# Kernel optimization log

Hardware: AMD Instinct MI355X
Metric: run time of the kernel (lower is better)

## Reference

```python
import jax, jax.numpy as jnp
import numpy as np

N = 262144      # total nodes in disjoint batch
E = 4194304     # total edges (COO)
G = 4096        # number of graphs
DIN = 1
CH = 32


def setup_inputs() -> dict:
    key = jax.random.key(0)
    ks = jax.random.split(key, 16)
    inp = {
        "x": jax.random.uniform(ks[0], (N, DIN), dtype=jnp.float32),
        "edge_src": jax.random.randint(ks[1], (E,), 0, N, dtype=jnp.int32),
        "edge_dst": jax.random.randint(ks[2], (E,), 0, N, dtype=jnp.int32),
        "edge_w": jax.random.uniform(ks[3], (E,), dtype=jnp.float32),  # normalized-adj values
        "seg": jnp.sort(jax.random.randint(ks[4], (N,), 0, G, dtype=jnp.int32)),
        "W1_1": jax.random.normal(ks[5], (DIN, CH), dtype=jnp.float32) * 0.5,
        "W2_1": jax.random.normal(ks[6], (DIN, CH), dtype=jnp.float32) * 0.5,
        "b1": jnp.zeros((CH,), jnp.float32),
        "W1_2": jax.random.normal(ks[7], (CH, CH), dtype=jnp.float32) * (1.0 / np.sqrt(CH)),
        "W2_2": jax.random.normal(ks[8], (CH, CH), dtype=jnp.float32) * (1.0 / np.sqrt(CH)),
        "b2": jnp.zeros((CH,), jnp.float32),
        "W1_3": jax.random.normal(ks[9], (CH, CH), dtype=jnp.float32) * (1.0 / np.sqrt(CH)),
        "W2_3": jax.random.normal(ks[10], (CH, CH), dtype=jnp.float32) * (1.0 / np.sqrt(CH)),
        "b3": jnp.zeros((CH,), jnp.float32),
        "Wd": jax.random.normal(ks[11], (CH, 1), dtype=jnp.float32) * (1.0 / np.sqrt(CH)),
        "bd": jnp.zeros((1,), jnp.float32),
    }
    return inp


def gcs_conv(x, src, dst, w, W1, W2, b):
    # GCSConv: out = relu(A_hat @ (x W1) + x W2 + b), A_hat sparse COO
    h = x @ W1                                   # [N, CH]
    msg = h[src] * w[:, None]                    # gather + edge weight [E, CH]
    agg = jax.ops.segment_sum(msg, dst, num_segments=N)  # scatter-add [N, CH]
    return jax.nn.relu(agg + x @ W2 + b)


def reference(x, edge_src, edge_dst, edge_w, seg,
              W1_1, W2_1, b1, W1_2, W2_2, b2, W1_3, W2_3, b3, Wd, bd):
    x = gcs_conv(x, edge_src, edge_dst, edge_w, W1_1, W2_1, b1)
    x = gcs_conv(x, edge_src, edge_dst, edge_w, W1_2, W2_2, b2)
    x = gcs_conv(x, edge_src, edge_dst, edge_w, W1_3, W2_3, b3)
    # GlobalAvgPool over graph segments
    sums = jax.ops.segment_sum(x, seg, num_segments=G)           # [G, CH]
    counts = jax.ops.segment_sum(jnp.ones((x.shape[0],), x.dtype), seg, num_segments=G)
    pooled = sums / jnp.maximum(counts, 1.0)[:, None]            # [G, CH]
    return jax.nn.sigmoid(pooled @ Wd + bd)                      # [G, 1]
```

## Files before the change

### kernel.cpp

```cpp
#include <hip/hip_runtime.h>
#include <hip/hip_bf16.h>

#define CH 32
#define BSHIFT 10
#define BNODES (1 << BSHIFT)
#define MAXBUK 256
#define P3_CHUNK 8192
#define NT 32
#define CAP 2048

__device__ __forceinline__ float bf_lo(unsigned int p) { return __int_as_float(p << 16); }
__device__ __forceinline__ float bf_hi(unsigned int p) { return __int_as_float(p & 0xffff0000u); }


__global__ void bucket_hist_kernel(const int* __restrict__ dst, int* __restrict__ bucketCount,
                                   int E, int nbuk) {
    __shared__ int h[MAXBUK];
    int tid = threadIdx.x;
    if (tid < nbuk) h[tid] = 0;
    __syncthreads();
    int stride = gridDim.x * blockDim.x;
    for (int e = blockIdx.x * blockDim.x + tid; e < E; e += stride)
        atomicAdd(&h[dst[e] >> BSHIFT], 1);
    __syncthreads();
    if (tid < nbuk && h[tid]) atomicAdd(&bucketCount[tid], h[tid]);
}

__global__ void bucket_scan_kernel(const int* __restrict__ bucketCount, int* __restrict__ bucketStart,
                                   int* __restrict__ bucketTail, int* __restrict__ row_start,
                                   int nbuk, int N, int E) {
    __shared__ int l[MAXBUK];
    int tid = threadIdx.x;
    int v = (tid < nbuk) ? bucketCount[tid] : 0;
    l[tid] = v;
    __syncthreads();
    for (int off = 1; off < MAXBUK; off <<= 1) {
        int t = (tid >= off) ? l[tid - off] : 0;
        __syncthreads();
        l[tid] += t;
        __syncthreads();
    }
    int ex = l[tid] - v;
    if (tid < nbuk) { bucketStart[tid] = ex; bucketTail[tid] = ex; }
    if (tid == nbuk - 1) bucketStart[nbuk] = ex + v;
    if (tid == 0) row_start[N] = E;
}

__global__ void bucket_scatter_kernel(const int* __restrict__ src, const int* __restrict__ dst,
                                      const float* __restrict__ w, int* __restrict__ bucketTail,
                                      int2* __restrict__ rec, int E, int nbuk) {
    __shared__ int cnt[MAXBUK], base[MAXBUK], offs[MAXBUK];
    int tid = threadIdx.x;
    int begin = blockIdx.x * P3_CHUNK;
    int end = min(begin + P3_CHUNK, E);
    if (tid < nbuk) cnt[tid] = 0;
    __syncthreads();
    for (int e = begin + tid; e < end; e += 256)
        atomicAdd(&cnt[dst[e] >> BSHIFT], 1);
    __syncthreads();
    if (tid < nbuk) {
        base[tid] = cnt[tid] ? atomicAdd(&bucketTail[tid], cnt[tid]) : 0;
        offs[tid] = 0;
    }
    __syncthreads();
    for (int e = begin + tid; e < end; e += 256) {
        int d = dst[e];
        int b = d >> BSHIFT;
        int p = base[b] + atomicAdd(&offs[b], 1);
        rec[p] = make_int2(src[e] | ((d & (BNODES - 1)) << 18), __float_as_int(w[e]));
    }
}

__global__ void local_csr_kernel(const int2* __restrict__ rec, const int* __restrict__ bucketStart,
                                 int* __restrict__ row_start, int2* __restrict__ colw, int N) {
    int b = blockIdx.x;
    int lo = bucketStart[b], hi = bucketStart[b + 1];
    int nodeBase = b << BSHIFT;
    int nNodes = min(BNODES, N - nodeBase);
    __shared__ int deg[BNODES];
    __shared__ int rs[BNODES];
    __shared__ int l[256];
    int tid = threadIdx.x;
    for (int i = tid; i < BNODES; i += 256) deg[i] = 0;
    __syncthreads();
    for (int j = lo + tid; j < hi; j += 256)
        atomicAdd(&deg[rec[j].x >> 18], 1);
    __syncthreads();
    int i0 = tid * 4;
    int v0 = deg[i0], v1 = deg[i0 + 1], v2 = deg[i0 + 2], v3 = deg[i0 + 3];
    int tsum = v0 + v1 + v2 + v3;
    l[tid] = tsum;
    __syncthreads();
    for (int off = 1; off < 256; off <<= 1) {
        int t = (tid >= off) ? l[tid - off] : 0;
        __syncthreads();
        l[tid] += t;
        __syncthreads();
    }
    int ex = l[tid] - tsum;
    rs[i0] = ex; rs[i0 + 1] = ex + v0; rs[i0 + 2] = ex + v0 + v1; rs[i0 + 3] = ex + v0 + v1 + v2;
    __syncthreads();
    for (int i = tid; i < nNodes; i += 256) row_start[nodeBase + i] = lo + rs[i];
    for (int i = tid; i < BNODES; i += 256) deg[i] = 0;
    __syncthreads();
    for (int j = lo + tid; j < hi; j += 256) {
        int2 r = rec[j];
        int dl = r.x >> 18;
        int p = lo + rs[dl] + atomicAdd(&deg[dl], 1);
        colw[p] = make_int2(r.x & 0x3FFFF, r.y);
    }
}

__global__ void l1_fused_kernel(const float* __restrict__ x,
                                const int* __restrict__ row_start, const int2* __restrict__ colw,
                                const float* __restrict__ W11, const float* __restrict__ W21,
                                const float* __restrict__ b1, const float* __restrict__ W12,
                                float* __restrict__ x1, __hip_bfloat16* __restrict__ h2, int N) {
    __shared__ float w1s[CH][CH];
    __shared__ float xs[8][CH + 1];
    int tid = threadIdx.x;
    for (int t = tid; t < CH * CH; t += 256) w1s[t >> 5][t & 31] = W12[t];
    int ln = tid >> 5, c = tid & 31;
    int node = blockIdx.x * 8 + ln;
    float s = 0.f, xv = 0.f;
    if (node < N) {
        xv = x[node];
        int lo = row_start[node], hi = row_start[node + 1];
        for (int j = lo + c; j < hi; j += 32) {
            int2 cw = colw[j];
            s += __int_as_float(cw.y) * x[cw.x];
        }
    }
    for (int m = 1; m < 32; m <<= 1) s += __shfl_xor(s, m);
    float x1v = 0.f;
    if (node < N) {
        x1v = fmaxf(fmaf(s, W11[c], fmaf(xv, W21[c], b1[c])), 0.f);
        x1[node * CH + c] = x1v;
    }
    xs[ln][c] = x1v;
    __syncthreads();
    if (node < N) {
        float a = 0.f;
#pragma unroll
        for (int k = 0; k < CH; k++) a = fmaf(xs[ln][k], w1s[k][c], a);
        h2[node * CH + c] = __float2bfloat16(a);
    }
}

__global__ void gemm_h_kernel(const float* __restrict__ xin, const float* __restrict__ W1,
                              __hip_bfloat16* __restrict__ h, int N) {
    __shared__ float w1s[CH][CH];
    __shared__ float xs[8][CH + 1];
    int tid = threadIdx.x;
    for (int t = tid; t < CH * CH; t += 256) w1s[t >> 5][t & 31] = W1[t];
    int ln = tid >> 5, c = tid & 31;
    int node = blockIdx.x * 8 + ln;
    float xv = (node < N) ? xin[node * CH + c] : 0.f;
    xs[ln][c] = xv;
    __syncthreads();
    if (node < N) {
        float a = 0.f;
#pragma unroll
        for (int k = 0; k < CH; k++) a = fmaf(xs[ln][k], w1s[k][c], a);
        h[node * CH + c] = __float2bfloat16(a);
    }
}

__global__ void gather_kernel(float* __restrict__ xio, const unsigned short* __restrict__ h,
                              const int* __restrict__ row_start, const int2* __restrict__ colw,
                              const float* __restrict__ W2, const float* __restrict__ b, int N) {
    __shared__ float w2s[CH][CH];
    __shared__ float xs[NT][CH + 1];
    __shared__ int2 cws[CAP];
    int tid = threadIdx.x;
    int nodeBase = blockIdx.x * NT;

    for (int t = tid; t < CH * CH; t += 256) w2s[t >> 5][t & 31] = W2[t];
    {
        int n = tid >> 5, c = tid & 31;
        for (int p = 0; p < NT / 8; p++) {
            int node = nodeBase + p * 8 + n;
            xs[p * 8 + n][c] = (node < N) ? xio[(size_t)node * CH + c] : 0.f;
        }
    }
    int tileEndNode = min(nodeBase + NT, N);
    int lo = row_start[min(nodeBase, N)];
    int hi = row_start[tileEndNode];
    int cnt = min(hi - lo, CAP);
    for (int t = tid; t < cnt; t += 256) cws[t] = colw[lo + t];
    __syncthreads();

    int grp = tid >> 4, l16 = tid & 15;
    int c0 = l16 * 2;
#pragma unroll
    for (int rep = 0; rep < NT / 16; rep++) {
        int nloc = rep * 16 + grp;
        int node = nodeBase + nloc;
        if (node >= N) continue;
        int ls = row_start[node], le = row_start[node + 1];
        float a0 = b[c0], a1 = b[c0 + 1];
#pragma unroll
        for (int k = 0; k < CH; k++) {
            float xk = xs[nloc][k];
            float2 wk = *reinterpret_cast<const float2*>(&w2s[k][c0]);
            a0 = fmaf(xk, wk.x, a0);
            a1 = fmaf(xk, wk.y, a1);
        }
        if (le - lo <= cnt) {
            int j = ls;
            for (; j + 4 <= le; j += 4) {
                int2 e0 = cws[j - lo], e1 = cws[j + 1 - lo], e2 = cws[j + 2 - lo], e3 = cws[j + 3 - lo];
                unsigned int p0 = *reinterpret_cast<const unsigned int*>(h + (size_t)e0.x * CH + c0);
                unsigned int p1 = *reinterpret_cast<const unsigned int*>(h + (size_t)e1.x * CH + c0);
                unsigned int p2 = *reinterpret_cast<const unsigned int*>(h + (size_t)e2.x * CH + c0);
                unsigned int p3 = *reinterpret_cast<const unsigned int*>(h + (size_t)e3.x * CH + c0);
                float w0 = __int_as_float(e0.y), w1 = __int_as_float(e1.y);
                float w2 = __int_as_float(e2.y), w3 = __int_as_float(e3.y);
                a0 = fmaf(w0, bf_lo(p0), a0); a1 = fmaf(w0, bf_hi(p0), a1);
                a0 = fmaf(w1, bf_lo(p1), a0); a1 = fmaf(w1, bf_hi(p1), a1);
                a0 = fmaf(w2, bf_lo(p2), a0); a1 = fmaf(w2, bf_hi(p2), a1);
                a0 = fmaf(w3, bf_lo(p3), a0); a1 = fmaf(w3, bf_hi(p3), a1);
            }
            for (; j < le; j++) {
                int2 e = cws[j - lo];
                unsigned int p = *reinterpret_cast<const unsigned int*>(h + (size_t)e.x * CH + c0);
                float wj = __int_as_float(e.y);
                a0 = fmaf(wj, bf_lo(p), a0); a1 = fmaf(wj, bf_hi(p), a1);
            }
        } else {
            for (int j = ls; j < le; j++) {
                int2 e = colw[j];
                unsigned int p = *reinterpret_cast<const unsigned int*>(h + (size_t)e.x * CH + c0);
                float wj = __int_as_float(e.y);
                a0 = fmaf(wj, bf_lo(p), a0); a1 = fmaf(wj, bf_hi(p), a1);
            }
        }
        float2 o = make_float2(fmaxf(a0, 0.f), fmaxf(a1, 0.f));
        *reinterpret_cast<float2*>(&xio[(size_t)node * CH + c0]) = o;
    }
}

__global__ void pool_head_kernel(const float* __restrict__ x3, const int* __restrict__ seg,
                                 const float* __restrict__ Wd, const float* __restrict__ bd,
                                 float* __restrict__ out, int N, int G) {
    int g = blockIdx.x;
    int tid = threadIdx.x;
    int lo = 0, hi = N;
    while (lo < hi) { int mid = (lo + hi) >> 1; if (seg[mid] < g) lo = mid + 1; else hi = mid; }
    int start = lo;
    hi = N;
    while (lo < hi) { int mid = (lo + hi) >> 1; if (seg[mid] < g + 1) lo = mid + 1; else hi = mid; }
    int end = lo;
    int half = tid >> 5, c = tid & 31;
    float s = 0.f;
    for (int n = start + half; n < end; n += 2) s += x3[(size_t)n * CH + c];
    s += __shfl_xor(s, 32);
    float t = s * Wd[c];
    for (int m = 1; m < 32; m <<= 1) t += __shfl_xor(t, m);
    if (tid == 0) {
        float cnt = fmaxf((float)(end - start), 1.f);
        float logit = t / cnt + bd[0];
        out[g] = 1.f / (1.f + expf(-logit));
    }
}

extern "C" void kernel_launch(void* const* d_in, const int* in_sizes, int n_in,
                              void* d_out, int out_size, void* d_ws, size_t ws_size,
                              hipStream_t stream) {
    const float* x        = (const float*)d_in[0];
    const int*   edge_src = (const int*)d_in[1];
    const int*   edge_dst = (const int*)d_in[2];
    const float* edge_w   = (const float*)d_in[3];
    const int*   seg      = (const int*)d_in[4];
    const float* W1_1 = (const float*)d_in[5];
    const float* W2_1 = (const float*)d_in[6];
    const float* b1   = (const float*)d_in[7];
    const float* W1_2 = (const float*)d_in[8];
    const float* W2_2 = (const float*)d_in[9];
    const float* b2   = (const float*)d_in[10];
    const float* W1_3 = (const float*)d_in[11];
    const float* W2_3 = (const float*)d_in[12];
    const float* b3   = (const float*)d_in[13];
    const float* Wd   = (const float*)d_in[14];
    const float* bd   = (const float*)d_in[15];
    float* out = (float*)d_out;

    const int N = in_sizes[0];
    const int E = in_sizes[1];
    const int G = out_size;
    (void)ws_size; (void)n_in;

    const int nbuk = (N + BNODES - 1) >> BSHIFT;

    const size_t NB = (size_t)N * CH;
    float*           xbuf      = (float*)d_ws;
    int2*            rec       = (int2*)d_ws;
    __hip_bfloat16*  h16       = (__hip_bfloat16*)(xbuf + NB);
    int*             row_start = (int*)(h16 + NB);
    int2*            colw      = (int2*)(row_start + (N + 8));
    int*             bucketCount = (int*)(colw + E);
    int*             bucketStart = bucketCount + MAXBUK;
    int*             bucketTail  = bucketStart + MAXBUK + 4;

    const int BLK = 256;

    hipMemsetAsync(bucketCount, 0, MAXBUK * sizeof(int), stream);
    bucket_hist_kernel<<<512, BLK, 0, stream>>>(edge_dst, bucketCount, E, nbuk);
    bucket_scan_kernel<<<1, BLK, 0, stream>>>(bucketCount, bucketStart, bucketTail, row_start, nbuk, N, E);
    bucket_scatter_kernel<<<(E + P3_CHUNK - 1) / P3_CHUNK, BLK, 0, stream>>>(
        edge_src, edge_dst, edge_w, bucketTail, rec, E, nbuk);
    local_csr_kernel<<<nbuk, BLK, 0, stream>>>(rec, bucketStart, row_start, colw, N);

    l1_fused_kernel<<<(N + 7) / 8, BLK, 0, stream>>>(x, row_start, colw,
                                                     W1_1, W2_1, b1, W1_2, xbuf, h16, N);
    gather_kernel<<<(N + NT - 1) / NT, BLK, 0, stream>>>(xbuf, (const unsigned short*)h16,
                                                         row_start, colw, W2_2, b2, N);
    gemm_h_kernel<<<(N + 7) / 8, BLK, 0, stream>>>(xbuf, W1_3, h16, N);
    gather_kernel<<<(N + NT - 1) / NT, BLK, 0, stream>>>(xbuf, (const unsigned short*)h16,
                                                         row_start, colw, W2_3, b3, N);

    pool_head_kernel<<<G, 64, 0, stream>>>(xbuf, seg, Wd, bd, out, N, G);
}
```

Measured before the change: 447.5 us.

## Store hidden features in FP8 and fuse next-layer GEMM into gather

Stores the per-node transformed features h in FP8 e4m3 instead of bf16, which halves the bytes fetched by the random per-edge gathers. The layer-2 gather kernel now also computes the layer-3 x@W1 product from its own outputs and writes it to a second h buffer, so the separate gemm_h kernel launch and its re-read of x go away. The edge-cache capacity CAP is lowered, which cuts shared memory and may raise occupancy. FP8 has far less mantissa than bf16, so accuracy drops and results could fail tolerance.

```diff
diff --git a/kernel.cpp b/kernel.cpp
--- a/kernel.cpp
+++ b/kernel.cpp
@@ -1,5 +1,6 @@
 #include <hip/hip_runtime.h>
 #include <hip/hip_bf16.h>
+#include <hip/hip_fp8.h>
 
 #define CH 32
 #define BSHIFT 10
@@ -7,10 +8,14 @@
 #define MAXBUK 256
 #define P3_CHUNK 8192
 #define NT 32
-#define CAP 2048
-
-__device__ __forceinline__ float bf_lo(unsigned int p) { return __int_as_float(p << 16); }
-__device__ __forceinline__ float bf_hi(unsigned int p) { return __int_as_float(p & 0xffff0000u); }
+#define CAP 1024
+
+__device__ __forceinline__ float fp8_to_f32(unsigned int b) {
+    __hip_fp8_e4m3 v; v.__x = (__hip_fp8_storage_t)b; return (float)v;
+}
+__device__ __forceinline__ unsigned char f32_to_fp8(float f) {
+    return (unsigned char)__hip_fp8_e4m3(f).__x;
+}
 
 
 __global__ void bucket_hist_kernel(const int* __restrict__ dst, int* __restrict__ bucketCount,
@@ -115,7 +120,7 @@
                                 const int* __restrict__ row_start, const int2* __restrict__ colw,
                                 const float* __restrict__ W11, const float* __restrict__ W21,
                                 const float* __restrict__ b1, const float* __restrict__ W12,
-                                float* __restrict__ x1, __hip_bfloat16* __restrict__ h2, int N) {
+                                float* __restrict__ x1, unsigned char* __restrict__ h2, int N) {
     __shared__ float w1s[CH][CH];
     __shared__ float xs[8][CH + 1];
     int tid = threadIdx.x;
@@ -135,7 +140,7 @@
     float x1v = 0.f;
     if (node < N) {
         x1v = fmaxf(fmaf(s, W11[c], fmaf(xv, W21[c], b1[c])), 0.f);
-        x1[node * CH + c] = x1v;
+        x1[(size_t)node * CH + c] = x1v;
     }
     xs[ln][c] = x1v;
     __syncthreads();
@@ -143,39 +148,27 @@
         float a = 0.f;
 #pragma unroll
         for (int k = 0; k < CH; k++) a = fmaf(xs[ln][k], w1s[k][c], a);
-        h2[node * CH + c] = __float2bfloat16(a);
-    }
-}
-
-__global__ void gemm_h_kernel(const float* __restrict__ xin, const float* __restrict__ W1,
-                              __hip_bfloat16* __restrict__ h, int N) {
-    __shared__ float w1s[CH][CH];
-    __shared__ float xs[8][CH + 1];
-    int tid = threadIdx.x;
-    for (int t = tid; t < CH * CH; t += 256) w1s[t >> 5][t & 31] = W1[t];
-    int ln = tid >> 5, c = tid & 31;
-    int node = blockIdx.x * 8 + ln;
-    float xv = (node < N) ? xin[node * CH + c] : 0.f;
-    xs[ln][c] = xv;
-    __syncthreads();
-    if (node < N) {
-        float a = 0.f;
-#pragma unroll
-        for (int k = 0; k < CH; k++) a = fmaf(xs[ln][k], w1s[k][c], a);
-        h[node * CH + c] = __float2bfloat16(a);
-    }
-}
-
-__global__ void gather_kernel(float* __restrict__ xio, const unsigned short* __restrict__ h,
+        h2[(size_t)node * CH + c] = f32_to_fp8(a);
+    }
+}
+
+template <bool EMIT_H>
+__global__ void gather_kernel(float* __restrict__ xio, const unsigned char* __restrict__ h,
                               const int* __restrict__ row_start, const int2* __restrict__ colw,
-                              const float* __restrict__ W2, const float* __restrict__ b, int N) {
+                              const float* __restrict__ W2, const float* __restrict__ b,
+                              const float* __restrict__ W1next, unsigned char* __restrict__ hout,
+                              int N) {
     __shared__ float w2s[CH][CH];
+    __shared__ float w1s[EMIT_H ? CH : 1][CH];
     __shared__ float xs[NT][CH + 1];
     __shared__ int2 cws[CAP];
     int tid = threadIdx.x;
     int nodeBase = blockIdx.x * NT;
 
-    for (int t = tid; t < CH * CH; t += 256) w2s[t >> 5][t & 31] = W2[t];
+    for (int t = tid; t < CH * CH; t += 256) {
+        w2s[t >> 5][t & 31] = W2[t];
+        if (EMIT_H) w1s[t >> 5][t & 31] = W1next[t];
+    }
     {
         int n = tid >> 5, c = tid & 31;
         for (int p = 0; p < NT / 8; p++) {
@@ -183,9 +176,8 @@
             xs[p * 8 + n][c] = (node < N) ? xio[(size_t)node * CH + c] : 0.f;
         }
     }
-    int tileEndNode = min(nodeBase + NT, N);
     int lo = row_start[min(nodeBase, N)];
-    int hi = row_start[tileEndNode];
+    int hi = row_start[min(nodeBase + NT, N)];
     int cnt = min(hi - lo, CAP);
     for (int t = tid; t < cnt; t += 256) cws[t] = colw[lo + t];
     __syncthreads();
@@ -196,47 +188,69 @@
     for (int rep = 0; rep < NT / 16; rep++) {
         int nloc = rep * 16 + grp;
         int node = nodeBase + nloc;
-        if (node >= N) continue;
-        int ls = row_start[node], le = row_start[node + 1];
-        float a0 = b[c0], a1 = b[c0 + 1];
-#pragma unroll
-        for (int k = 0; k < CH; k++) {
-            float xk = xs[nloc][k];
-            float2 wk = *reinterpret_cast<const float2*>(&w2s[k][c0]);
-            a0 = fmaf(xk, wk.x, a0);
-            a1 = fmaf(xk, wk.y, a1);
+        if (node < N) {
+            int ls = row_start[node], le = row_start[node + 1];
+            float a0 = b[c0], a1 = b[c0 + 1];
+#pragma unroll
+            for (int k = 0; k < CH; k++) {
+                float xk = xs[nloc][k];
+                float2 wk = *reinterpret_cast<const float2*>(&w2s[k][c0]);
+                a0 = fmaf(xk, wk.x, a0);
+                a1 = fmaf(xk, wk.y, a1);
+            }
+            if (le - lo <= cnt) {
+                int j = ls;
+                for (; j + 4 <= le; j += 4) {
+                    int2 e0 = cws[j - lo], e1 = cws[j + 1 - lo], e2 = cws[j + 2 - lo], e3 = cws[j + 3 - lo];
+                    unsigned int p0 = *reinterpret_cast<const unsigned short*>(h + (size_t)e0.x * CH + c0);
+                    unsigned int p1 = *reinterpret_cast<const unsigned short*>(h + (size_t)e1.x * CH + c0);
+                    unsigned int p2 = *reinterpret_cast<const unsigned short*>(h + (size_t)e2.x * CH + c0);
+                    unsigned int p3 = *reinterpret_cast<const unsigned short*>(h + (size_t)e3.x * CH + c0);
+                    float w0 = __int_as_float(e0.y), w1 = __int_as_float(e1.y);
+                    float w2 = __int_as_float(e2.y), w3 = __int_as_float(e3.y);
+                    a0 = fmaf(w0, fp8_to_f32(p0 & 0xff), a0); a1 = fmaf(w0, fp8_to_f32(p0 >> 8), a1);
+                    a0 = fmaf(w1, fp8_to_f32(p1 & 0xff), a0); a1 = fmaf(w1, fp8_to_f32(p1 >> 8), a1);
+                    a0 = fmaf(w2, fp8_to_f32(p2 & 0xff), a0); a1 = fmaf(w2, fp8_to_f32(p2 >> 8), a1);
+                    a0 = fmaf(w3, fp8_to_f32(p3 & 0xff), a0); a1 = fmaf(w3, fp8_to_f32(p3 >> 8), a1);
+                }
+                for (; j < le; j++) {
+                    int2 e = cws[j - lo];
+                    unsigned int p = *reinterpret_cast<const unsigned short*>(h + (size_t)e.x * CH + c0);
+                    float wj = __int_as_float(e.y);
+                    a0 = fmaf(wj, fp8_to_f32(p & 0xff), a0); a1 = fmaf(wj, fp8_to_f32(p >> 8), a1);
+                }
+            } else {
+                for (int j = ls; j < le; j++) {
+                    int2 e = colw[j];
+                    unsigned int p = *reinterpret_cast<const unsigned short*>(h + (size_t)e.x * CH + c0);
+                    float wj = __int_as_float(e.y);
+                    a0 = fmaf(wj, fp8_to_f32(p & 0xff), a0); a1 = fmaf(wj, fp8_to_f32(p >> 8), a1);
+                }
+            }
+            float r0 = fmaxf(a0, 0.f), r1 = fmaxf(a1, 0.f);
+            *reinterpret_cast<float2*>(&xio[(size_t)node * CH + c0]) = make_float2(r0, r1);
+            if (EMIT_H) { xs[nloc][c0] = r0; xs[nloc][c0 + 1] = r1; }
         }
-        if (le - lo <= cnt) {
-            int j = ls;
-            for (; j + 4 <= le; j += 4) {
-                int2 e0 = cws[j - lo], e1 = cws[j + 1 - lo], e2 = cws[j + 2 - lo], e3 = cws[j + 3 - lo];
-                unsigned int p0 = *reinterpret_cast<const unsigned int*>(h + (size_t)e0.x * CH + c0);
-                unsigned int p1 = *reinterpret_cast<const unsigned int*>(h + (size_t)e1.x * CH + c0);
-                unsigned int p2 = *reinterpret_cast<const unsigned int*>(h + (size_t)e2.x * CH + c0);
-                unsigned int p3 = *reinterpret_cast<const unsigned int*>(h + (size_t)e3.x * CH + c0);
-                float w0 = __int_as_float(e0.y), w1 = __int_as_float(e1.y);
-                float w2 = __int_as_float(e2.y), w3 = __int_as_float(e3.y);
-                a0 = fmaf(w0, bf_lo(p0), a0); a1 = fmaf(w0, bf_hi(p0), a1);
-                a0 = fmaf(w1, bf_lo(p1), a0); a1 = fmaf(w1, bf_hi(p1), a1);
-                a0 = fmaf(w2, bf_lo(p2), a0); a1 = fmaf(w2, bf_hi(p2), a1);
-                a0 = fmaf(w3, bf_lo(p3), a0); a1 = fmaf(w3, bf_hi(p3), a1);
+    }
+    if (EMIT_H) {
+        __syncthreads();
+#pragma unroll
+        for (int rep = 0; rep < NT / 16; rep++) {
+            int nloc = rep * 16 + grp;
+            int node = nodeBase + nloc;
+            if (node >= N) continue;
+            float a0 = 0.f, a1 = 0.f;
+#pragma unroll
+            for (int k = 0; k < CH; k++) {
+                float xk = xs[nloc][k];
+                float2 wk = *reinterpret_cast<const float2*>(&w1s[k][c0]);
+                a0 = fmaf(xk, wk.x, a0);
+                a1 = fmaf(xk, wk.y, a1);
             }
-            for (; j < le; j++) {
-                int2 e = cws[j - lo];
-                unsigned int p = *reinterpret_cast<const unsigned int*>(h + (size_t)e.x * CH + c0);
-                float wj = __int_as_float(e.y);
-                a0 = fmaf(wj, bf_lo(p), a0); a1 = fmaf(wj, bf_hi(p), a1);
-            }
-        } else {
-            for (int j = ls; j < le; j++) {
-                int2 e = colw[j];
-                unsigned int p = *reinterpret_cast<const unsigned int*>(h + (size_t)e.x * CH + c0);
-                float wj = __int_as_float(e.y);
-                a0 = fmaf(wj, bf_lo(p), a0); a1 = fmaf(wj, bf_hi(p), a1);
-            }
+            unsigned short pk = (unsigned short)f32_to_fp8(a0) |
+                                ((unsigned short)f32_to_fp8(a1) << 8);
+            *reinterpret_cast<unsigned short*>(hout + (size_t)node * CH + c0) = pk;
         }
-        float2 o = make_float2(fmaxf(a0, 0.f), fmaxf(a1, 0.f));
-        *reinterpret_cast<float2*>(&xio[(size_t)node * CH + c0]) = o;
     }
 }
 
@@ -295,8 +309,9 @@
     const size_t NB = (size_t)N * CH;
     float*           xbuf      = (float*)d_ws;
     int2*            rec       = (int2*)d_ws;
-    __hip_bfloat16*  h16       = (__hip_bfloat16*)(xbuf + NB);
-    int*             row_start = (int*)(h16 + NB);
+    unsigned char*   h8a       = (unsigned char*)(xbuf + NB);
+    unsigned char*   h8b       = h8a + NB;
+    int*             row_start = (int*)(h8b + NB);
     int2*            colw      = (int2*)(row_start + (N + 8));
     int*             bucketCount = (int*)(colw + E);
     int*             bucketStart = bucketCount + MAXBUK;
@@ -312,12 +327,11 @@
     local_csr_kernel<<<nbuk, BLK, 0, stream>>>(rec, bucketStart, row_start, colw, N);
 
     l1_fused_kernel<<<(N + 7) / 8, BLK, 0, stream>>>(x, row_start, colw,
-                                                     W1_1, W2_1, b1, W1_2, xbuf, h16, N);
-    gather_kernel<<<(N + NT - 1) / NT, BLK, 0, stream>>>(xbuf, (const unsigned short*)h16,
-                                                         row_start, colw, W2_2, b2, N);
-    gemm_h_kernel<<<(N + 7) / 8, BLK, 0, stream>>>(xbuf, W1_3, h16, N);
-    gather_kernel<<<(N + NT - 1) / NT, BLK, 0, stream>>>(xbuf, (const unsigned short*)h16,
-                                                         row_start, colw, W2_3, b3, N);
+                                                     W1_1, W2_1, b1, W1_2, xbuf, h8a, N);
+    gather_kernel<true><<<(N + NT - 1) / NT, BLK, 0, stream>>>(xbuf, h8a, row_start, colw,
+                                                               W2_2, b2, W1_3, h8b, N);
+    gather_kernel<false><<<(N + NT - 1) / NT, BLK, 0, stream>>>(xbuf, h8b, row_start, colw,
+                                                                W2_3, b3, nullptr, nullptr, N);
 
     pool_head_kernel<<<G, 64, 0, stream>>>(xbuf, seg, Wd, bd, out, N, G);
 }
```

Result: faster. 411.7 us (-8.0%).

## Store gathered features as FP8 and split aggregation into two channel-half passes

Applied to the files above, without the earlier changes.

The per-node message table h changes from bf16 to FP8 e4m3 and is stored as two 16-channel half tables. Each gather layer now runs as two passes, one per half. The first pass computes the x·W2+bias seed for all channels and stashes the upper half in xio for the second pass. Halving the table width should shrink the random-gather working set (N*16 bytes per half) so it fits better in cache, at the cost of an extra launch, rereading edges twice, and much lower precision in the aggregated messages.

```diff
diff --git a/kernel.cpp b/kernel.cpp
--- a/kernel.cpp
+++ b/kernel.cpp
@@ -1,16 +1,22 @@
 #include <hip/hip_runtime.h>
 #include <hip/hip_bf16.h>
+#include <hip/hip_fp8.h>
 
 #define CH 32
+#define HCH 16
 #define BSHIFT 10
 #define BNODES (1 << BSHIFT)
 #define MAXBUK 256
 #define P3_CHUNK 8192
 #define NT 32
-#define CAP 2048
-
-__device__ __forceinline__ float bf_lo(unsigned int p) { return __int_as_float(p << 16); }
-__device__ __forceinline__ float bf_hi(unsigned int p) { return __int_as_float(p & 0xffff0000u); }
+#define CAP 768
+
+__device__ __forceinline__ float fp8_to_f32(unsigned int b) {
+    __hip_fp8_e4m3 v; v.__x = (__hip_fp8_storage_t)b; return (float)v;
+}
+__device__ __forceinline__ unsigned char f32_to_fp8(float f) {
+    return (unsigned char)__hip_fp8_e4m3(f).__x;
+}
 
 
 __global__ void bucket_hist_kernel(const int* __restrict__ dst, int* __restrict__ bucketCount,
@@ -115,7 +121,8 @@
                                 const int* __restrict__ row_start, const int2* __restrict__ colw,
                                 const float* __restrict__ W11, const float* __restrict__ W21,
                                 const float* __restrict__ b1, const float* __restrict__ W12,
-                                float* __restrict__ x1, __hip_bfloat16* __restrict__ h2, int N) {
+                                float* __restrict__ x1,
+                                unsigned char* __restrict__ hlo, unsigned char* __restrict__ hhi, int N) {
     __shared__ float w1s[CH][CH];
     __shared__ float xs[8][CH + 1];
     int tid = threadIdx.x;
@@ -128,14 +135,14 @@
         int lo = row_start[node], hi = row_start[node + 1];
         for (int j = lo + c; j < hi; j += 32) {
             int2 cw = colw[j];
-            s += __int_as_float(cw.y) * x[cw.x];
+            s += __int_as_float(cw.y) * x[cw.x & 0x3FFFF];
         }
     }
     for (int m = 1; m < 32; m <<= 1) s += __shfl_xor(s, m);
     float x1v = 0.f;
     if (node < N) {
         x1v = fmaxf(fmaf(s, W11[c], fmaf(xv, W21[c], b1[c])), 0.f);
-        x1[node * CH + c] = x1v;
+        x1[(size_t)node * CH + c] = x1v;
     }
     xs[ln][c] = x1v;
     __syncthreads();
@@ -143,100 +150,123 @@
         float a = 0.f;
 #pragma unroll
         for (int k = 0; k < CH; k++) a = fmaf(xs[ln][k], w1s[k][c], a);
-        h2[node * CH + c] = __float2bfloat16(a);
+        if (c < HCH) hlo[(size_t)node * HCH + c] = f32_to_fp8(a);
+        else         hhi[(size_t)node * HCH + (c - HCH)] = f32_to_fp8(a);
     }
 }
 
 __global__ void gemm_h_kernel(const float* __restrict__ xin, const float* __restrict__ W1,
-                              __hip_bfloat16* __restrict__ h, int N) {
+                              unsigned char* __restrict__ hlo, unsigned char* __restrict__ hhi, int N) {
     __shared__ float w1s[CH][CH];
     __shared__ float xs[8][CH + 1];
     int tid = threadIdx.x;
     for (int t = tid; t < CH * CH; t += 256) w1s[t >> 5][t & 31] = W1[t];
     int ln = tid >> 5, c = tid & 31;
     int node = blockIdx.x * 8 + ln;
-    float xv = (node < N) ? xin[node * CH + c] : 0.f;
+    float xv = (node < N) ? xin[(size_t)node * CH + c] : 0.f;
     xs[ln][c] = xv;
     __syncthreads();
     if (node < N) {
         float a = 0.f;
 #pragma unroll
         for (int k = 0; k < CH; k++) a = fmaf(xs[ln][k], w1s[k][c], a);
-        h[node * CH + c] = __float2bfloat16(a);
-    }
-}
-
-__global__ void gather_kernel(float* __restrict__ xio, const unsigned short* __restrict__ h,
-                              const int* __restrict__ row_start, const int2* __restrict__ colw,
-                              const float* __restrict__ W2, const float* __restrict__ b, int N) {
-    __shared__ float w2s[CH][CH];
-    __shared__ float xs[NT][CH + 1];
+        if (c < HCH) hlo[(size_t)node * HCH + c] = f32_to_fp8(a);
+        else         hhi[(size_t)node * HCH + (c - HCH)] = f32_to_fp8(a);
+    }
+}
+
+template <bool SEED>
+__global__ void gather_half_kernel(float* __restrict__ xio, const unsigned char* __restrict__ tab,
+                                   const int* __restrict__ row_start, const int2* __restrict__ colw,
+                                   const float* __restrict__ W2, const float* __restrict__ bias,
+                                   int N) {
+    __shared__ float w2s[SEED ? CH : 1][CH];
+    __shared__ float xs[SEED ? NT : 1][CH + 1];
     __shared__ int2 cws[CAP];
+    const int co = SEED ? 0 : HCH;
     int tid = threadIdx.x;
     int nodeBase = blockIdx.x * NT;
-
-    for (int t = tid; t < CH * CH; t += 256) w2s[t >> 5][t & 31] = W2[t];
-    {
-        int n = tid >> 5, c = tid & 31;
-        for (int p = 0; p < NT / 8; p++) {
-            int node = nodeBase + p * 8 + n;
-            xs[p * 8 + n][c] = (node < N) ? xio[(size_t)node * CH + c] : 0.f;
-        }
-    }
-    int tileEndNode = min(nodeBase + NT, N);
+    int n = tid >> 3, l8 = tid & 7;
+    int node = nodeBase + n;
+    int cc = l8 * 2;
+
+    if (SEED) {
+        for (int t = tid; t < CH * CH; t += 256) w2s[t >> 5][t & 31] = W2[t];
+        int c0 = l8 * 4;
+        float4 xv = make_float4(0.f, 0.f, 0.f, 0.f);
+        if (node < N) xv = *reinterpret_cast<const float4*>(&xio[(size_t)node * CH + c0]);
+        xs[n][c0] = xv.x; xs[n][c0 + 1] = xv.y; xs[n][c0 + 2] = xv.z; xs[n][c0 + 3] = xv.w;
+    }
     int lo = row_start[min(nodeBase, N)];
-    int hi = row_start[tileEndNode];
-    int cnt = min(hi - lo, CAP);
+    int hi = row_start[min(nodeBase + NT, N)];
+    int total = hi - lo;
+    int cnt = min(total, CAP);
     for (int t = tid; t < cnt; t += 256) cws[t] = colw[lo + t];
     __syncthreads();
 
-    int grp = tid >> 4, l16 = tid & 15;
-    int c0 = l16 * 2;
-#pragma unroll
-    for (int rep = 0; rep < NT / 16; rep++) {
-        int nloc = rep * 16 + grp;
-        int node = nodeBase + nloc;
-        if (node >= N) continue;
-        int ls = row_start[node], le = row_start[node + 1];
-        float a0 = b[c0], a1 = b[c0 + 1];
+    float acc0, acc1;
+    if (SEED) {
+        int c0 = l8 * 4;
+        float a0 = bias[c0], a1 = bias[c0 + 1], a2 = bias[c0 + 2], a3 = bias[c0 + 3];
 #pragma unroll
         for (int k = 0; k < CH; k++) {
-            float xk = xs[nloc][k];
-            float2 wk = *reinterpret_cast<const float2*>(&w2s[k][c0]);
+            float xk = xs[n][k];
+            float4 wk = *reinterpret_cast<const float4*>(&w2s[k][c0]);
             a0 = fmaf(xk, wk.x, a0);
             a1 = fmaf(xk, wk.y, a1);
-        }
-        if (le - lo <= cnt) {
-            int j = ls;
-            for (; j + 4 <= le; j += 4) {
-                int2 e0 = cws[j - lo], e1 = cws[j + 1 - lo], e2 = cws[j + 2 - lo], e3 = cws[j + 3 - lo];
-                unsigned int p0 = *reinterpret_cast<const unsigned int*>(h + (size_t)e0.x * CH + c0);
-                unsigned int p1 = *reinterpret_cast<const unsigned int*>(h + (size_t)e1.x * CH + c0);
-                unsigned int p2 = *reinterpret_cast<const unsigned int*>(h + (size_t)e2.x * CH + c0);
-                unsigned int p3 = *reinterpret_cast<const unsigned int*>(h + (size_t)e3.x * CH + c0);
-                float w0 = __int_as_float(e0.y), w1 = __int_as_float(e1.y);
-                float w2 = __int_as_float(e2.y), w3 = __int_as_float(e3.y);
-                a0 = fmaf(w0, bf_lo(p0), a0); a1 = fmaf(w0, bf_hi(p0), a1);
-                a0 = fmaf(w1, bf_lo(p1), a0); a1 = fmaf(w1, bf_hi(p1), a1);
-                a0 = fmaf(w2, bf_lo(p2), a0); a1 = fmaf(w2, bf_hi(p2), a1);
-                a0 = fmaf(w3, bf_lo(p3), a0); a1 = fmaf(w3, bf_hi(p3), a1);
-            }
-            for (; j < le; j++) {
-                int2 e = cws[j - lo];
-                unsigned int p = *reinterpret_cast<const unsigned int*>(h + (size_t)e.x * CH + c0);
-                float wj = __int_as_float(e.y);
-                a0 = fmaf(wj, bf_lo(p), a0); a1 = fmaf(wj, bf_hi(p), a1);
-            }
+            a2 = fmaf(xk, wk.z, a2);
+            a3 = fmaf(xk, wk.w, a3);
+        }
+        __syncthreads();
+        if (c0 >= HCH) {
+            if (node < N)
+                *reinterpret_cast<float4*>(&xio[(size_t)node * CH + c0]) = make_float4(a0, a1, a2, a3);
         } else {
-            for (int j = ls; j < le; j++) {
-                int2 e = colw[j];
-                unsigned int p = *reinterpret_cast<const unsigned int*>(h + (size_t)e.x * CH + c0);
-                float wj = __int_as_float(e.y);
-                a0 = fmaf(wj, bf_lo(p), a0); a1 = fmaf(wj, bf_hi(p), a1);
-            }
-        }
-        float2 o = make_float2(fmaxf(a0, 0.f), fmaxf(a1, 0.f));
-        *reinterpret_cast<float2*>(&xio[(size_t)node * CH + c0]) = o;
+            xs[n][c0] = a0; xs[n][c0 + 1] = a1; xs[n][c0 + 2] = a2; xs[n][c0 + 3] = a3;
+        }
+        __syncthreads();
+        acc0 = xs[n][cc]; acc1 = xs[n][cc + 1];
+    } else {
+        float2 sd = make_float2(0.f, 0.f);
+        if (node < N) sd = *reinterpret_cast<const float2*>(&xio[(size_t)node * CH + co + cc]);
+        acc0 = sd.x; acc1 = sd.y;
+    }
+
+    int ls = (node < N) ? row_start[node] : 0;
+    int le = (node < N) ? row_start[node + 1] : 0;
+    const unsigned char* tp = tab + cc;
+    if (total <= cnt) {
+        int j = ls;
+        for (; j + 4 <= le; j += 4) {
+            int2 e0 = cws[j - lo], e1 = cws[j + 1 - lo], e2 = cws[j + 2 - lo], e3 = cws[j + 3 - lo];
+            unsigned int p0 = *reinterpret_cast<const unsigned short*>(tp + (size_t)(e0.x & 0x3FFFF) * HCH);
+            unsigned int p1 = *reinterpret_cast<const unsigned short*>(tp + (size_t)(e1.x & 0x3FFFF) * HCH);
+            unsigned int p2 = *reinterpret_cast<const unsigned short*>(tp + (size_t)(e2.x & 0x3FFFF) * HCH);
+            unsigned int p3 = *reinterpret_cast<const unsigned short*>(tp + (size_t)(e3.x & 0x3FFFF) * HCH);
+            float w0 = __int_as_float(e0.y), w1 = __int_as_float(e1.y);
+            float w2 = __int_as_float(e2.y), w3 = __int_as_float(e3.y);
+            acc0 = fmaf(w0, fp8_to_f32(p0 & 0xff), acc0); acc1 = fmaf(w0, fp8_to_f32(p0 >> 8), acc1);
+            acc0 = fmaf(w1, fp8_to_f32(p1 & 0xff), acc0); acc1 = fmaf(w1, fp8_to_f32(p1 >> 8), acc1);
+            acc0 = fmaf(w2, fp8_to_f32(p2 & 0xff), acc0); acc1 = fmaf(w2, fp8_to_f32(p2 >> 8), acc1);
+            acc0 = fmaf(w3, fp8_to_f32(p3 & 0xff), acc0); acc1 = fmaf(w3, fp8_to_f32(p3 >> 8), acc1);
+        }
+        for (; j < le; j++) {
+            int2 e = cws[j - lo];
+            unsigned int p = *reinterpret_cast<const unsigned short*>(tp + (size_t)(e.x & 0x3FFFF) * HCH);
+            float wj = __int_as_float(e.y);
+            acc0 = fmaf(wj, fp8_to_f32(p & 0xff), acc0); acc1 = fmaf(wj, fp8_to_f32(p >> 8), acc1);
+        }
+    } else {
+        for (int j = ls; j < le; j++) {
+            int2 e = colw[j];
+            unsigned int p = *reinterpret_cast<const unsigned short*>(tp + (size_t)(e.x & 0x3FFFF) * HCH);
+            float wj = __int_as_float(e.y);
+            acc0 = fmaf(wj, fp8_to_f32(p & 0xff), acc0); acc1 = fmaf(wj, fp8_to_f32(p >> 8), acc1);
+        }
+    }
+    if (node < N) {
+        *reinterpret_cast<float2*>(&xio[(size_t)node * CH + co + cc]) =
+            make_float2(fmaxf(acc0, 0.f), fmaxf(acc1, 0.f));
     }
 }
 
@@ -253,13 +283,13 @@
     int end = lo;
     int half = tid >> 5, c = tid & 31;
     float s = 0.f;
-    for (int n = start + half; n < end; n += 2) s += x3[(size_t)n * CH + c];
+    for (int nn = start + half; nn < end; nn += 2) s += x3[(size_t)nn * CH + c];
     s += __shfl_xor(s, 32);
     float t = s * Wd[c];
     for (int m = 1; m < 32; m <<= 1) t += __shfl_xor(t, m);
     if (tid == 0) {
-        float cnt = fmaxf((float)(end - start), 1.f);
-        float logit = t / cnt + bd[0];
+        float cntf = fmaxf((float)(end - start), 1.f);
+        float logit = t / cntf + bd[0];
         out[g] = 1.f / (1.f + expf(-logit));
     }
 }
@@ -293,10 +323,14 @@
     const int nbuk = (N + BNODES - 1) >> BSHIFT;
 
     const size_t NB = (size_t)N * CH;
+    const size_t NH = (size_t)N * HCH;
     float*           xbuf      = (float*)d_ws;
     int2*            rec       = (int2*)d_ws;
-    __hip_bfloat16*  h16       = (__hip_bfloat16*)(xbuf + NB);
-    int*             row_start = (int*)(h16 + NB);
+    unsigned char*   h2lo      = (unsigned char*)(xbuf + NB);
+    unsigned char*   h2hi      = h2lo + NH;
+    unsigned char*   h3lo      = h2hi + NH;
+    unsigned char*   h3hi      = h3lo + NH;
+    int*             row_start = (int*)(h3hi + NH);
     int2*            colw      = (int2*)(row_start + (N + 8));
     int*             bucketCount = (int*)(colw + E);
     int*             bucketStart = bucketCount + MAXBUK;
@@ -312,12 +346,12 @@
     local_csr_kernel<<<nbuk, BLK, 0, stream>>>(rec, bucketStart, row_start, colw, N);
 
     l1_fused_kernel<<<(N + 7) / 8, BLK, 0, stream>>>(x, row_start, colw,
-                                                     W1_1, W2_1, b1, W1_2, xbuf, h16, N);
-    gather_kernel<<<(N + NT - 1) / NT, BLK, 0, stream>>>(xbuf, (const unsigned short*)h16,
-                                                         row_start, colw, W2_2, b2, N);
-    gemm_h_kernel<<<(N + 7) / 8, BLK, 0, stream>>>(xbuf, W1_3, h16, N);
-    gather_kernel<<<(N + NT - 1) / NT, BLK, 0, stream>>>(xbuf, (const unsigned short*)h16,
-                                                         row_start, colw, W2_3, b3, N);
+                                                     W1_1, W2_1, b1, W1_2, xbuf, h2lo, h2hi, N);
+    gather_half_kernel<true><<<(N + NT - 1) / NT, BLK, 0, stream>>>(xbuf, h2lo, row_start, colw, W2_2, b2, N);
+    gather_half_kernel<false><<<(N + NT - 1) / NT, BLK, 0, stream>>>(xbuf, h2hi, row_start, colw, W2_2, b2, N);
+    gemm_h_kernel<<<(N + 7) / 8, BLK, 0, stream>>>(xbuf, W1_3, h3lo, h3hi, N);
+    gather_half_kernel<true><<<(N + NT - 1) / NT, BLK, 0, stream>>>(xbuf, h3lo, row_start, colw, W2_3, b3, N);
+    gather_half_kernel<false><<<(N + NT - 1) / NT, BLK, 0, stream>>>(xbuf, h3hi, row_start, colw, W2_3, b3, N);
 
     pool_head_kernel<<<G, 64, 0, stream>>>(xbuf, seg, Wd, bd, out, N, G);
 }
```

Measured after the change: 446.3 us. No clear change (-0.3%).
